# Kernel optimization log

Measured on AMD Instinct MI355X. Metric: run time of the kernel, lower is better.

## Reference

```python
import jax, jax.numpy as jnp
import numpy as np

N_PATHS = 8
T2_EFF = 0.5 * 100.0 + 0.5 * (100 // 50)  # p_dimer*T2_dimer + p_trimer*T2_trimer = 51.0
J_FREQ = 20.0


def setup_inputs() -> dict:
    key = jax.random.key(0)
    ks = jax.random.split(key, 5)
    B, D, H, P = 2048, 1024, 1024, N_PATHS
    return {
        "x": jax.random.normal(ks[0], (B, D), dtype=jnp.float32),
        "W_input": jax.random.normal(ks[1], (D, H), dtype=jnp.float32) * 0.1,
        "W_paths": jax.random.normal(ks[2], (P, H, H), dtype=jnp.float32) * 0.1,
        "J_coupling": jax.random.normal(ks[3], (P, P), dtype=jnp.float32) * 0.01,
        "coherent_state": jax.random.normal(ks[4], (B, P, H), dtype=jnp.float32),
        "t": jnp.ones((1,), dtype=jnp.float32),  # time_since_formation buffer
    }


def reference(x, W_input, W_paths, J_coupling, coherent_state, t):
    # base activation: [B, H]
    base = x @ W_input
    # all per-path matmuls batched into one einsum: [B, P, H]
    path_act = jnp.einsum("bh,phk->bpk", base, W_paths)
    # coherence decay gate (scalar, broadcasts)
    alpha = jnp.clip(jnp.exp(-t[0] / T2_EFF), 0.0, 1.0)
    superposition = alpha * coherent_state + (1.0 - alpha) * path_act
    # interference matrix from symmetrized J-coupling
    J_sym = 0.5 * (J_coupling + J_coupling.T)
    phase = 2.0 * jnp.pi * J_FREQ * t[0] / 1000.0
    interference = jax.nn.softmax(jnp.cos(phase * J_sym), axis=1)  # [P, P]
    # double-loop mixing == small matmul over path dim
    interfered = jnp.einsum("ij,bjh->bih", interference, superposition) / N_PATHS
    interfered = interfered * alpha  # coherence_factor == alpha
    # no measurement (default path): mean over paths
    return jnp.mean(interfered, axis=1)  # [B, H]
```

## Files before the change

kernel.cpp:

```cpp
#include <hip/hip_runtime.h>
#include <cstdint>


typedef __attribute__((ext_vector_type(8))) __bf16 bf16x8;
typedef __attribute__((ext_vector_type(4))) float f32x4;
typedef unsigned short u16;

__device__ __forceinline__ u16 f32_to_bf16_rne(float f) {
  unsigned int u = __float_as_uint(f);
  u += 0x7fffu + ((u >> 16) & 1u);
  return (u16)(u >> 16);
}

__device__ __forceinline__ f32x4 nt_load4(const float* p) {
  return __builtin_nontemporal_load((const f32x4*)p);
}

__device__ __forceinline__ void wave_scalars(const float* __restrict__ J,
                                             const float* __restrict__ t,
                                             float* w_out, float* alpha_out) {
  const int lane = threadIdx.x & 63;
  float tv = t[0];
  float alpha = fminf(fmaxf(expf(-tv / 51.0f), 0.0f), 1.0f);
  float phase = 2.0f * 3.14159265358979323846f * 20.0f * tv / 1000.0f;
  int i = lane >> 3, j = lane & 7;
  float jsym = 0.5f * (J[i * 8 + j] + J[j * 8 + i]);
  float e = expf(cosf(phase * jsym));
  float rs = e;
  rs += __shfl_xor(rs, 1);
  rs += __shfl_xor(rs, 2);
  rs += __shfl_xor(rs, 4);
  float p = e / rs;
  float cs = p;
  cs += __shfl_xor(cs, 8);
  cs += __shfl_xor(cs, 16);
  cs += __shfl_xor(cs, 32);
  *w_out = alpha * (1.0f / 64.0f) * cs;
  *alpha_out = alpha;
}

__global__ __launch_bounds__(256, 4) void k_prep(
    const float* __restrict__ x, const float* __restrict__ win,
    const float* __restrict__ wp, const float* __restrict__ J,
    const float* __restrict__ t, u16* __restrict__ xfrag,
    u16* __restrict__ winfrag, u16* __restrict__ wefrag) {
  __shared__ __align__(16) char smem[33024];
  const int blk = blockIdx.x;
  const int tid = threadIdx.x;
  const int lane = tid & 63;

  if (blk < 512) {
    float* lt = (float*)smem;
    float wv, alpha;
    wave_scalars(J, t, &wv, &alpha);
    float wLO[8];
#pragma unroll
    for (int p = 0; p < 8; p++)
      wLO[p] = __shfl(wv, (lane & 56) | p) * (1.0f - alpha);
    const int a0 = (blk & 31) * 32;
    const int b0 = (blk >> 5) * 64;
    f32x4 v[2][8];
#pragma unroll
    for (int s = 0; s < 2; s++) {
      const int item = s * 256 + tid;
      const int row = item >> 4, ch = item & 15;
      const float* base = wp + (size_t)(a0 + row) * 1024 + b0 + ch * 4;
#pragma unroll
      for (int j = 0; j < 8; j++) v[s][j] = nt_load4(base + (size_t)j * 1048576);
    }
#pragma unroll
    for (int s = 0; s < 2; s++) {
      const int item = s * 256 + tid;
      const int row = item >> 4, ch = item & 15;
      f32x4 acc = {0.f, 0.f, 0.f, 0.f};
#pragma unroll
      for (int j = 0; j < 8; j++) acc += wLO[j] * v[s][j];
      *(f32x4*)&lt[row * 68 + ch * 4] = acc;
    }
    __syncthreads();
    {
      const int lf = tid & 63, rtl = tid >> 6;
      const int rowh2 = rtl * 16 + (lf & 15);
      const int kh1 = (lf >> 4) << 3;
      __align__(16) u16 o[8];
#pragma unroll
      for (int i = 0; i < 8; i++)
        o[i] = f32_to_bf16_rne(lt[(kh1 + i) * 68 + rowh2]);
      const int rt = (b0 >> 4) + rtl, kt = a0 >> 5;
      *(uint4*)(wefrag + ((size_t)(rt * 32 + kt) * 64 + lf) * 8) = *(const uint4*)o;
    }
  } else {
    const int cid = blk - 512;
    const float* src;
    u16* dst;
    if (cid < 128) {
      src = x + (size_t)cid * 16384;
      dst = xfrag + (size_t)cid * 16384;
    } else {
      src = win + (size_t)(cid - 128) * 16384;
      dst = winfrag + (size_t)(cid - 128) * 16384;
    }
    u16* ld = (u16*)smem;
    f32x4 v[16];
#pragma unroll
    for (int row = 0; row < 16; row++) v[row] = nt_load4(src + row * 1024 + tid * 4);
#pragma unroll
    for (int row = 0; row < 16; row++) {
      ushort4 o;
      o.x = f32_to_bf16_rne(v[row][0]);
      o.y = f32_to_bf16_rne(v[row][1]);
      o.z = f32_to_bf16_rne(v[row][2]);
      o.w = f32_to_bf16_rne(v[row][3]);
      *(ushort4*)(ld + row * 1032 + tid * 4) = o;
    }
    __syncthreads();
#pragma unroll
    for (int s = 0; s < 8; s++) {
      int idx = s * 256 + tid;
      int lf = idx & 63, kt = idx >> 6;
      int row = lf & 15, colb = kt * 32 + ((lf >> 4) << 3);
      *(uint4*)(dst + (kt * 64 + lf) * 8) = *(const uint4*)(ld + row * 1032 + colb);
    }
  }
}

__global__ __launch_bounds__(256, 4) void k_gemm0(const u16* __restrict__ Af,
                                                  const u16* __restrict__ Bf,
                                                  u16* __restrict__ ofrag) {
  __shared__ u16 ct[64 * 36];
  const int tid = threadIdx.x;
  const int wave = tid >> 6, lane = tid & 63;
  const int quad = lane >> 4, t16 = lane & 15;
  const int m0 = blockIdx.x * 64;
  const int n0 = blockIdx.y * 32;
  const u16* ap = Af + ((size_t)((m0 + wave * 16) >> 4) * 32) * 512 + lane * 8;
  const u16* bp = Bf + ((size_t)(n0 >> 4) * 32) * 512 + lane * 8;

  f32x4 acc[2] = {{0.f, 0.f, 0.f, 0.f}, {0.f, 0.f, 0.f, 0.f}};
  for (int kb = 0; kb < 32; kb += 4) {
    bf16x8 a[4], b0[4], b1[4];
#pragma unroll
    for (int u = 0; u < 4; u++) {
      a[u] = *(const bf16x8*)(ap + (kb + u) * 512);
      b0[u] = *(const bf16x8*)(bp + (kb + u) * 512);
      b1[u] = *(const bf16x8*)(bp + (32 + kb + u) * 512);
    }
#pragma unroll
    for (int u = 0; u < 4; u++) {
      acc[0] = __builtin_amdgcn_mfma_f32_16x16x32_bf16(a[u], b0[u], acc[0], 0, 0, 0);
      acc[1] = __builtin_amdgcn_mfma_f32_16x16x32_bf16(a[u], b1[u], acc[1], 0, 0, 0);
    }
  }
#pragma unroll
  for (int r = 0; r < 4; r++)
#pragma unroll
    for (int ni = 0; ni < 2; ni++)
      ct[(wave * 16 + quad * 4 + r) * 36 + ni * 16 + t16] =
          f32_to_bf16_rne(acc[ni][r]);
  __syncthreads();
  {
    int lf = tid & 63, rtl = tid >> 6;
    int rowl = rtl * 16 + (lf & 15);
    int colb = (lf >> 4) << 3;
    __align__(16) u16 o[8];
#pragma unroll
    for (int i = 0; i < 8; i++) o[i] = ct[rowl * 36 + colb + i];
    *(uint4*)(ofrag +
              ((size_t)(((m0 >> 4) + rtl) * 32 + (n0 >> 5)) * 64 + lf) * 8) =
        *(const uint4*)o;
  }
}

__global__ __launch_bounds__(512, 4) void k_main(
    const u16* __restrict__ Af, const u16* __restrict__ Bf,
    const float* __restrict__ coh, const float* __restrict__ J,
    const float* __restrict__ t, float* __restrict__ out) {
  __shared__ float cs_lds[64 * 68];
  const int tid = threadIdx.x;
  const int wave = tid >> 6, lane = tid & 63;
  const int m0 = blockIdx.x * 64;
  const int n0 = blockIdx.y * 64;
  const int quad = lane >> 4, t16 = lane & 15;
  const int wm = (wave >> 1) * 32, wn = (wave & 1) * 32;

  f32x4 acc[2][2];
  if (wave < 4) {
    const u16* ap = Af + ((size_t)((m0 + wm) >> 4) * 32) * 512 + lane * 8;
    const u16* bp = Bf + ((size_t)((n0 + wn) >> 4) * 32) * 512 + lane * 8;
#pragma unroll
    for (int mi = 0; mi < 2; mi++)
#pragma unroll
      for (int ni = 0; ni < 2; ni++) acc[mi][ni] = (f32x4){0.f, 0.f, 0.f, 0.f};
    for (int kb = 0; kb < 32; kb += 4) {
      bf16x8 a0[4], a1[4], b0[4], b1[4];
#pragma unroll
      for (int u = 0; u < 4; u++) {
        a0[u] = *(const bf16x8*)(ap + (kb + u) * 512);
        a1[u] = *(const bf16x8*)(ap + (32 + kb + u) * 512);
        b0[u] = *(const bf16x8*)(bp + (kb + u) * 512);
        b1[u] = *(const bf16x8*)(bp + (32 + kb + u) * 512);
      }
#pragma unroll
      for (int u = 0; u < 4; u++) {
        acc[0][0] = __builtin_amdgcn_mfma_f32_16x16x32_bf16(a0[u], b0[u], acc[0][0], 0, 0, 0);
        acc[0][1] = __builtin_amdgcn_mfma_f32_16x16x32_bf16(a0[u], b1[u], acc[0][1], 0, 0, 0);
        acc[1][0] = __builtin_amdgcn_mfma_f32_16x16x32_bf16(a1[u], b0[u], acc[1][0], 0, 0, 0);
        acc[1][1] = __builtin_amdgcn_mfma_f32_16x16x32_bf16(a1[u], b1[u], acc[1][1], 0, 0, 0);
      }
    }
  } else {
    float wv, alpha;
    wave_scalars(J, t, &wv, &alpha);
    float wHI[8];
#pragma unroll
    for (int p = 0; p < 8; p++) wHI[p] = __shfl(wv, (lane & 56) | p) * alpha;
    const int tc = (wave - 4) * 64 + lane;
    const int c4 = tc & 15;
    const int rb = tc >> 4;
    const float* cb = coh + (size_t)m0 * 8192 + n0 + c4 * 4;
#pragma unroll
    for (int up = 0; up < 2; up++) {
      f32x4 v[2][8];
#pragma unroll
      for (int h = 0; h < 2; h++) {
        const float* cr = cb + (size_t)(rb + 16 * (up * 2 + h)) * 8192;
#pragma unroll
        for (int p = 0; p < 8; p++) v[h][p] = nt_load4(cr + p * 1024);
      }
#pragma unroll
      for (int h = 0; h < 2; h++) {
        f32x4 a4 = {0.f, 0.f, 0.f, 0.f};
#pragma unroll
        for (int p = 0; p < 8; p++) a4 += wHI[p] * v[h][p];
        *(f32x4*)&cs_lds[(rb + 16 * (up * 2 + h)) * 68 + c4 * 4] = a4;
      }
    }
  }
  __syncthreads();
  if (wave < 4) {
#pragma unroll
    for (int mi = 0; mi < 2; mi++)
#pragma unroll
      for (int r = 0; r < 4; r++) {
        const int ml = wm + mi * 16 + quad * 4 + r;
        const size_t mrow = (size_t)(m0 + ml) * 1024;
#pragma unroll
        for (int ni = 0; ni < 2; ni++) {
          const int nl = wn + ni * 16 + t16;
          out[mrow + n0 + nl] = acc[mi][ni][r] + cs_lds[ml * 68 + nl];
        }
      }
  }
}

extern "C" void kernel_launch(void* const* d_in, const int* in_sizes, int n_in,
                              void* d_out, int out_size, void* d_ws, size_t ws_size,
                              hipStream_t stream) {
  const float* x   = (const float*)d_in[0];
  const float* win = (const float*)d_in[1];
  const float* wp  = (const float*)d_in[2];
  const float* J   = (const float*)d_in[3];
  const float* coh = (const float*)d_in[4];
  const float* t   = (const float*)d_in[5];
  float* out = (float*)d_out;

  char* ws = (char*)d_ws;
  u16* xfrag   = (u16*)ws;
  u16* winfrag = (u16*)(ws + 4u * 1024 * 1024);
  u16* wefrag  = (u16*)(ws + 6u * 1024 * 1024);
  u16* wctfrag = (u16*)(ws + 8u * 1024 * 1024);

  k_prep<<<704, 256, 0, stream>>>(x, win, wp, J, t, xfrag, winfrag, wefrag);
  k_gemm0<<<dim3(16, 32), 256, 0, stream>>>(wefrag, winfrag, wctfrag);
  k_main<<<dim3(32, 16), 512, 0, stream>>>(xfrag, wctfrag, coh, J, t, out);
}
```

Measured before the change: 158.6 us.

## Move x conversion into gemm0 kernel and swizzle blocks across XCDs

New measurement: 157.1 us. About the same (-1.0%).

```diff
diff --git a/kernel.cpp b/kernel.cpp
--- a/kernel.cpp
+++ b/kernel.cpp
@@ -39,10 +39,34 @@
   *alpha_out = alpha;
 }
 
+__device__ __forceinline__ void convert16(const float* __restrict__ src,
+                                          u16* __restrict__ dst, u16* ld,
+                                          int tid) {
+  f32x4 v[16];
+#pragma unroll
+  for (int row = 0; row < 16; row++) v[row] = nt_load4(src + row * 1024 + tid * 4);
+#pragma unroll
+  for (int row = 0; row < 16; row++) {
+    ushort4 o;
+    o.x = f32_to_bf16_rne(v[row][0]);
+    o.y = f32_to_bf16_rne(v[row][1]);
+    o.z = f32_to_bf16_rne(v[row][2]);
+    o.w = f32_to_bf16_rne(v[row][3]);
+    *(ushort4*)(ld + row * 1032 + tid * 4) = o;
+  }
+  __syncthreads();
+#pragma unroll
+  for (int s = 0; s < 8; s++) {
+    int idx = s * 256 + tid;
+    int lf = idx & 63, kt = idx >> 6;
+    int row = lf & 15, colb = kt * 32 + ((lf >> 4) << 3);
+    *(uint4*)(dst + (kt * 64 + lf) * 8) = *(const uint4*)(ld + row * 1032 + colb);
+  }
+}
+
 __global__ __launch_bounds__(256, 4) void k_prep(
-    const float* __restrict__ x, const float* __restrict__ win,
-    const float* __restrict__ wp, const float* __restrict__ J,
-    const float* __restrict__ t, u16* __restrict__ xfrag,
+    const float* __restrict__ win, const float* __restrict__ wp,
+    const float* __restrict__ J, const float* __restrict__ t,
     u16* __restrict__ winfrag, u16* __restrict__ wefrag) {
   __shared__ __align__(16) char smem[33024];
   const int blk = blockIdx.x;
@@ -91,83 +115,66 @@
     }
   } else {
     const int cid = blk - 512;
-    const float* src;
-    u16* dst;
-    if (cid < 128) {
-      src = x + (size_t)cid * 16384;
-      dst = xfrag + (size_t)cid * 16384;
-    } else {
-      src = win + (size_t)(cid - 128) * 16384;
-      dst = winfrag + (size_t)(cid - 128) * 16384;
-    }
-    u16* ld = (u16*)smem;
-    f32x4 v[16];
-#pragma unroll
-    for (int row = 0; row < 16; row++) v[row] = nt_load4(src + row * 1024 + tid * 4);
-#pragma unroll
-    for (int row = 0; row < 16; row++) {
-      ushort4 o;
-      o.x = f32_to_bf16_rne(v[row][0]);
-      o.y = f32_to_bf16_rne(v[row][1]);
-      o.z = f32_to_bf16_rne(v[row][2]);
-      o.w = f32_to_bf16_rne(v[row][3]);
-      *(ushort4*)(ld + row * 1032 + tid * 4) = o;
-    }
+    convert16(win + (size_t)cid * 16384, winfrag + (size_t)cid * 16384,
+              (u16*)smem, tid);
+  }
+}
+
+__global__ __launch_bounds__(256, 4) void k_mid(
+    const float* __restrict__ x, const u16* __restrict__ Af,
+    const u16* __restrict__ Bf, u16* __restrict__ xfrag,
+    u16* __restrict__ ofrag) {
+  __shared__ __align__(16) char smem[33024];
+  const int blk = blockIdx.x;
+  const int tid = threadIdx.x;
+
+  if (blk < 512) {
+    u16* ct = (u16*)smem;
+    const int wave = tid >> 6, lane = tid & 63;
+    const int quad = lane >> 4, t16 = lane & 15;
+    const int xcd = blk & 7, i = blk >> 3;
+    const int m0 = (xcd + 8 * (i & 1)) * 64;
+    const int n0 = (i >> 1) * 32;
+    const u16* ap = Af + ((size_t)((m0 + wave * 16) >> 4) * 32) * 512 + lane * 8;
+    const u16* bp = Bf + ((size_t)(n0 >> 4) * 32) * 512 + lane * 8;
+
+    f32x4 acc[2] = {{0.f, 0.f, 0.f, 0.f}, {0.f, 0.f, 0.f, 0.f}};
+    for (int kb = 0; kb < 32; kb += 4) {
+      bf16x8 a[4], b0[4], b1[4];
+#pragma unroll
+      for (int u = 0; u < 4; u++) {
+        a[u] = *(const bf16x8*)(ap + (kb + u) * 512);
+        b0[u] = *(const bf16x8*)(bp + (kb + u) * 512);
+        b1[u] = *(const bf16x8*)(bp + (32 + kb + u) * 512);
+      }
+#pragma unroll
+      for (int u = 0; u < 4; u++) {
+        acc[0] = __builtin_amdgcn_mfma_f32_16x16x32_bf16(a[u], b0[u], acc[0], 0, 0, 0);
+        acc[1] = __builtin_amdgcn_mfma_f32_16x16x32_bf16(a[u], b1[u], acc[1], 0, 0, 0);
+      }
+    }
+#pragma unroll
+    for (int r = 0; r < 4; r++)
+#pragma unroll
+      for (int ni = 0; ni < 2; ni++)
+        ct[(wave * 16 + quad * 4 + r) * 36 + ni * 16 + t16] =
+            f32_to_bf16_rne(acc[ni][r]);
     __syncthreads();
-#pragma unroll
-    for (int s = 0; s < 8; s++) {
-      int idx = s * 256 + tid;
-      int lf = idx & 63, kt = idx >> 6;
-      int row = lf & 15, colb = kt * 32 + ((lf >> 4) << 3);
-      *(uint4*)(dst + (kt * 64 + lf) * 8) = *(const uint4*)(ld + row * 1032 + colb);
-    }
-  }
-}
-
-__global__ __launch_bounds__(256, 4) void k_gemm0(const u16* __restrict__ Af,
-                                                  const u16* __restrict__ Bf,
-                                                  u16* __restrict__ ofrag) {
-  __shared__ u16 ct[64 * 36];
-  const int tid = threadIdx.x;
-  const int wave = tid >> 6, lane = tid & 63;
-  const int quad = lane >> 4, t16 = lane & 15;
-  const int m0 = blockIdx.x * 64;
-  const int n0 = blockIdx.y * 32;
-  const u16* ap = Af + ((size_t)((m0 + wave * 16) >> 4) * 32) * 512 + lane * 8;
-  const u16* bp = Bf + ((size_t)(n0 >> 4) * 32) * 512 + lane * 8;
-
-  f32x4 acc[2] = {{0.f, 0.f, 0.f, 0.f}, {0.f, 0.f, 0.f, 0.f}};
-  for (int kb = 0; kb < 32; kb += 4) {
-    bf16x8 a[4], b0[4], b1[4];
-#pragma unroll
-    for (int u = 0; u < 4; u++) {
-      a[u] = *(const bf16x8*)(ap + (kb + u) * 512);
-      b0[u] = *(const bf16x8*)(bp + (kb + u) * 512);
-      b1[u] = *(const bf16x8*)(bp + (32 + kb + u) * 512);
-    }
-#pragma unroll
-    for (int u = 0; u < 4; u++) {
-      acc[0] = __builtin_amdgcn_mfma_f32_16x16x32_bf16(a[u], b0[u], acc[0], 0, 0, 0);
-      acc[1] = __builtin_amdgcn_mfma_f32_16x16x32_bf16(a[u], b1[u], acc[1], 0, 0, 0);
-    }
-  }
-#pragma unroll
-  for (int r = 0; r < 4; r++)
-#pragma unroll
-    for (int ni = 0; ni < 2; ni++)
-      ct[(wave * 16 + quad * 4 + r) * 36 + ni * 16 + t16] =
-          f32_to_bf16_rne(acc[ni][r]);
-  __syncthreads();
-  {
-    int lf = tid & 63, rtl = tid >> 6;
-    int rowl = rtl * 16 + (lf & 15);
-    int colb = (lf >> 4) << 3;
-    __align__(16) u16 o[8];
-#pragma unroll
-    for (int i = 0; i < 8; i++) o[i] = ct[rowl * 36 + colb + i];
-    *(uint4*)(ofrag +
-              ((size_t)(((m0 >> 4) + rtl) * 32 + (n0 >> 5)) * 64 + lf) * 8) =
-        *(const uint4*)o;
+    {
+      int lf = tid & 63, rtl = tid >> 6;
+      int rowl = rtl * 16 + (lf & 15);
+      int colb = (lf >> 4) << 3;
+      __align__(16) u16 o[8];
+#pragma unroll
+      for (int i2 = 0; i2 < 8; i2++) o[i2] = ct[rowl * 36 + colb + i2];
+      *(uint4*)(ofrag +
+                ((size_t)(((m0 >> 4) + rtl) * 32 + (n0 >> 5)) * 64 + lf) * 8) =
+          *(const uint4*)o;
+    }
+  } else {
+    const int cid = blk - 512;
+    convert16(x + (size_t)cid * 16384, xfrag + (size_t)cid * 16384, (u16*)smem,
+              tid);
   }
 }
 
@@ -178,8 +185,9 @@
   __shared__ float cs_lds[64 * 68];
   const int tid = threadIdx.x;
   const int wave = tid >> 6, lane = tid & 63;
-  const int m0 = blockIdx.x * 64;
-  const int n0 = blockIdx.y * 64;
+  const int xcd = blockIdx.x & 7, i = blockIdx.x >> 3;
+  const int m0 = (xcd + 8 * (i >> 4)) * 64;
+  const int n0 = (i & 15) * 64;
   const int quad = lane >> 4, t16 = lane & 15;
   const int wm = (wave >> 1) * 32, wn = (wave & 1) * 32;
 
@@ -270,7 +278,7 @@
   u16* wefrag  = (u16*)(ws + 6u * 1024 * 1024);
   u16* wctfrag = (u16*)(ws + 8u * 1024 * 1024);
 
-  k_prep<<<704, 256, 0, stream>>>(x, win, wp, J, t, xfrag, winfrag, wefrag);
-  k_gemm0<<<dim3(16, 32), 256, 0, stream>>>(wefrag, winfrag, wctfrag);
-  k_main<<<dim3(32, 16), 512, 0, stream>>>(xfrag, wctfrag, coh, J, t, out);
-}
+  k_prep<<<576, 256, 0, stream>>>(win, wp, J, t, winfrag, wefrag);
+  k_mid<<<640, 256, 0, stream>>>(x, wefrag, winfrag, xfrag, wctfrag);
+  k_main<<<512, 512, 0, stream>>>(xfrag, wctfrag, coh, J, t, out);
+}
```

## Fuse prep and both GEMMs into one persistent kernel with grid barriers

Applied to the files above, without the earlier changes.

New measurement: 354.7 us. 124% more time.

```diff
diff --git a/kernel.cpp b/kernel.cpp
--- a/kernel.cpp
+++ b/kernel.cpp
@@ -12,9 +12,7 @@
   return (u16)(u >> 16);
 }
 
-__device__ __forceinline__ f32x4 nt_load4(const float* p) {
-  return __builtin_nontemporal_load((const f32x4*)p);
-}
+__device__ __forceinline__ f32x4 ld4(const float* p) { return *(const f32x4*)p; }
 
 __device__ __forceinline__ void wave_scalars(const float* __restrict__ J,
                                              const float* __restrict__ t,
@@ -39,217 +37,229 @@
   *alpha_out = alpha;
 }
 
-__global__ __launch_bounds__(256, 4) void k_prep(
+__device__ __forceinline__ void grid_barrier(unsigned* cnt, unsigned target) {
+  __syncthreads();
+  __threadfence();
+  if (threadIdx.x == 0) {
+    __hip_atomic_fetch_add(cnt, 1u, __ATOMIC_ACQ_REL, __HIP_MEMORY_SCOPE_AGENT);
+    while (__hip_atomic_load(cnt, __ATOMIC_RELAXED, __HIP_MEMORY_SCOPE_AGENT) <
+           target)
+      __builtin_amdgcn_s_sleep(2);
+  }
+  __syncthreads();
+  __threadfence();
+}
+
+__global__ __launch_bounds__(512, 4) void k_fused(
     const float* __restrict__ x, const float* __restrict__ win,
     const float* __restrict__ wp, const float* __restrict__ J,
-    const float* __restrict__ t, u16* __restrict__ xfrag,
-    u16* __restrict__ winfrag, u16* __restrict__ wefrag) {
+    const float* __restrict__ t, const float* __restrict__ coh,
+    u16* __restrict__ xfrag, u16* __restrict__ winfrag,
+    u16* __restrict__ wefrag, u16* __restrict__ wctfrag,
+    float* __restrict__ out, unsigned* __restrict__ cnt) {
   __shared__ __align__(16) char smem[33024];
   const int blk = blockIdx.x;
   const int tid = threadIdx.x;
-  const int lane = tid & 63;
-
-  if (blk < 512) {
+  const int wave = tid >> 6, lane = tid & 63;
+  const int quad = lane >> 4, t16 = lane & 15;
+
+  float wv, alpha;
+  wave_scalars(J, t, &wv, &alpha);
+  float wLO[8], wHI[8];
+#pragma unroll
+  for (int p = 0; p < 8; p++) {
+    float wj = __shfl(wv, (lane & 56) | p);
+    wLO[p] = wj * (1.0f - alpha);
+    wHI[p] = wj * alpha;
+  }
+
+  {
     float* lt = (float*)smem;
-    float wv, alpha;
-    wave_scalars(J, t, &wv, &alpha);
-    float wLO[8];
-#pragma unroll
-    for (int p = 0; p < 8; p++)
-      wLO[p] = __shfl(wv, (lane & 56) | p) * (1.0f - alpha);
-    const int a0 = (blk & 31) * 32;
-    const int b0 = (blk >> 5) * 64;
+    const int row = tid >> 4, ch = tid & 15;
     f32x4 v[2][8];
 #pragma unroll
-    for (int s = 0; s < 2; s++) {
-      const int item = s * 256 + tid;
-      const int row = item >> 4, ch = item & 15;
+    for (int u = 0; u < 2; u++) {
+      const int tau = 2 * blk + u;
+      const int a0 = (tau & 31) * 32, b0 = (tau >> 5) * 64;
       const float* base = wp + (size_t)(a0 + row) * 1024 + b0 + ch * 4;
 #pragma unroll
-      for (int j = 0; j < 8; j++) v[s][j] = nt_load4(base + (size_t)j * 1048576);
-    }
-#pragma unroll
-    for (int s = 0; s < 2; s++) {
-      const int item = s * 256 + tid;
-      const int row = item >> 4, ch = item & 15;
+      for (int j = 0; j < 8; j++) v[u][j] = ld4(base + (size_t)j * 1048576);
+    }
+#pragma unroll
+    for (int u = 0; u < 2; u++) {
       f32x4 acc = {0.f, 0.f, 0.f, 0.f};
 #pragma unroll
-      for (int j = 0; j < 8; j++) acc += wLO[j] * v[s][j];
-      *(f32x4*)&lt[row * 68 + ch * 4] = acc;
+      for (int j = 0; j < 8; j++) acc += wLO[j] * v[u][j];
+      *(f32x4*)&lt[(u * 32 + row) * 68 + ch * 4] = acc;
     }
     __syncthreads();
     {
-      const int lf = tid & 63, rtl = tid >> 6;
+      const int u = tid >> 8, utid = tid & 255;
+      const int lf = utid & 63, rtl = utid >> 6;
+      const int tau = 2 * blk + u;
+      const int a0 = (tau & 31) * 32, b0 = (tau >> 5) * 64;
       const int rowh2 = rtl * 16 + (lf & 15);
       const int kh1 = (lf >> 4) << 3;
       __align__(16) u16 o[8];
 #pragma unroll
       for (int i = 0; i < 8; i++)
-        o[i] = f32_to_bf16_rne(lt[(kh1 + i) * 68 + rowh2]);
-      const int rt = (b0 >> 4) + rtl, kt = a0 >> 5;
-      *(uint4*)(wefrag + ((size_t)(rt * 32 + kt) * 64 + lf) * 8) = *(const uint4*)o;
-    }
-  } else {
-    const int cid = blk - 512;
+        o[i] = f32_to_bf16_rne(lt[(u * 32 + kh1 + i) * 68 + rowh2]);
+      *(uint4*)(wefrag +
+                ((size_t)(((b0 >> 4) + rtl) * 32 + (a0 >> 5)) * 64 + lf) * 8) =
+          *(const uint4*)o;
+    }
+    __syncthreads();
+  }
+
+  if (blk < 192) {
     const float* src;
     u16* dst;
-    if (cid < 128) {
-      src = x + (size_t)cid * 16384;
-      dst = xfrag + (size_t)cid * 16384;
+    if (blk < 128) {
+      src = x + (size_t)blk * 16384;
+      dst = xfrag + (size_t)blk * 16384;
     } else {
-      src = win + (size_t)(cid - 128) * 16384;
-      dst = winfrag + (size_t)(cid - 128) * 16384;
+      src = win + (size_t)(blk - 128) * 16384;
+      dst = winfrag + (size_t)(blk - 128) * 16384;
     }
     u16* ld = (u16*)smem;
-    f32x4 v[16];
-#pragma unroll
-    for (int row = 0; row < 16; row++) v[row] = nt_load4(src + row * 1024 + tid * 4);
-#pragma unroll
-    for (int row = 0; row < 16; row++) {
+    f32x4 v[8];
+#pragma unroll
+    for (int s = 0; s < 8; s++) {
+      int u2 = s * 512 + tid;
+      v[s] = ld4(src + (u2 >> 8) * 1024 + (u2 & 255) * 4);
+    }
+#pragma unroll
+    for (int s = 0; s < 8; s++) {
+      int u2 = s * 512 + tid;
       ushort4 o;
-      o.x = f32_to_bf16_rne(v[row][0]);
-      o.y = f32_to_bf16_rne(v[row][1]);
-      o.z = f32_to_bf16_rne(v[row][2]);
-      o.w = f32_to_bf16_rne(v[row][3]);
-      *(ushort4*)(ld + row * 1032 + tid * 4) = o;
-    }
-    __syncthreads();
-#pragma unroll
-    for (int s = 0; s < 8; s++) {
-      int idx = s * 256 + tid;
+      o.x = f32_to_bf16_rne(v[s][0]);
+      o.y = f32_to_bf16_rne(v[s][1]);
+      o.z = f32_to_bf16_rne(v[s][2]);
+      o.w = f32_to_bf16_rne(v[s][3]);
+      *(ushort4*)(ld + (u2 >> 8) * 1032 + (u2 & 255) * 4) = o;
+    }
+    __syncthreads();
+#pragma unroll
+    for (int s = 0; s < 4; s++) {
+      int idx = s * 512 + tid;
       int lf = idx & 63, kt = idx >> 6;
       int row = lf & 15, colb = kt * 32 + ((lf >> 4) << 3);
       *(uint4*)(dst + (kt * 64 + lf) * 8) = *(const uint4*)(ld + row * 1032 + colb);
     }
   }
-}
-
-__global__ __launch_bounds__(256, 4) void k_gemm0(const u16* __restrict__ Af,
-                                                  const u16* __restrict__ Bf,
-                                                  u16* __restrict__ ofrag) {
-  __shared__ u16 ct[64 * 36];
-  const int tid = threadIdx.x;
-  const int wave = tid >> 6, lane = tid & 63;
-  const int quad = lane >> 4, t16 = lane & 15;
-  const int m0 = blockIdx.x * 64;
-  const int n0 = blockIdx.y * 32;
-  const u16* ap = Af + ((size_t)((m0 + wave * 16) >> 4) * 32) * 512 + lane * 8;
-  const u16* bp = Bf + ((size_t)(n0 >> 4) * 32) * 512 + lane * 8;
-
-  f32x4 acc[2] = {{0.f, 0.f, 0.f, 0.f}, {0.f, 0.f, 0.f, 0.f}};
-  for (int kb = 0; kb < 32; kb += 4) {
-    bf16x8 a[4], b0[4], b1[4];
-#pragma unroll
-    for (int u = 0; u < 4; u++) {
-      a[u] = *(const bf16x8*)(ap + (kb + u) * 512);
-      b0[u] = *(const bf16x8*)(bp + (kb + u) * 512);
-      b1[u] = *(const bf16x8*)(bp + (32 + kb + u) * 512);
-    }
-#pragma unroll
-    for (int u = 0; u < 4; u++) {
-      acc[0] = __builtin_amdgcn_mfma_f32_16x16x32_bf16(a[u], b0[u], acc[0], 0, 0, 0);
-      acc[1] = __builtin_amdgcn_mfma_f32_16x16x32_bf16(a[u], b1[u], acc[1], 0, 0, 0);
-    }
-  }
-#pragma unroll
-  for (int r = 0; r < 4; r++)
-#pragma unroll
-    for (int ni = 0; ni < 2; ni++)
-      ct[(wave * 16 + quad * 4 + r) * 36 + ni * 16 + t16] =
-          f32_to_bf16_rne(acc[ni][r]);
-  __syncthreads();
+
+#pragma unroll
+  for (int half = 0; half < 2; half++) {
+    f32x4 v[2][8];
+    float* outp[2];
+#pragma unroll
+    for (int c = 0; c < 2; c++) {
+      const int cc = half * 2 + c;
+      const int u = cc >> 1, q = cc & 1;
+      const int tau = 2 * blk + u;
+      const int m0 = (tau >> 4) * 64, n0 = (tau & 15) * 64;
+      const int unit = q * 512 + tid;
+      const int row = unit >> 4, ch = unit & 15;
+      const float* cb = coh + (size_t)(m0 + row) * 8192 + n0 + ch * 4;
+#pragma unroll
+      for (int p = 0; p < 8; p++) v[c][p] = ld4(cb + p * 1024);
+      outp[c] = out + (size_t)(m0 + row) * 1024 + n0 + ch * 4;
+    }
+#pragma unroll
+    for (int c = 0; c < 2; c++) {
+      f32x4 a = {0.f, 0.f, 0.f, 0.f};
+#pragma unroll
+      for (int p = 0; p < 8; p++) a += wHI[p] * v[c][p];
+      *(f32x4*)outp[c] = a;
+    }
+  }
+
+  grid_barrier(cnt, 256);
+
   {
-    int lf = tid & 63, rtl = tid >> 6;
-    int rowl = rtl * 16 + (lf & 15);
-    int colb = (lf >> 4) << 3;
-    __align__(16) u16 o[8];
-#pragma unroll
-    for (int i = 0; i < 8; i++) o[i] = ct[rowl * 36 + colb + i];
-    *(uint4*)(ofrag +
-              ((size_t)(((m0 >> 4) + rtl) * 32 + (n0 >> 5)) * 64 + lf) * 8) =
-        *(const uint4*)o;
-  }
-}
-
-__global__ __launch_bounds__(512, 4) void k_main(
-    const u16* __restrict__ Af, const u16* __restrict__ Bf,
-    const float* __restrict__ coh, const float* __restrict__ J,
-    const float* __restrict__ t, float* __restrict__ out) {
-  __shared__ float cs_lds[64 * 68];
-  const int tid = threadIdx.x;
-  const int wave = tid >> 6, lane = tid & 63;
-  const int m0 = blockIdx.x * 64;
-  const int n0 = blockIdx.y * 64;
-  const int quad = lane >> 4, t16 = lane & 15;
-  const int wm = (wave >> 1) * 32, wn = (wave & 1) * 32;
-
-  f32x4 acc[2][2];
-  if (wave < 4) {
-    const u16* ap = Af + ((size_t)((m0 + wm) >> 4) * 32) * 512 + lane * 8;
-    const u16* bp = Bf + ((size_t)((n0 + wn) >> 4) * 32) * 512 + lane * 8;
-#pragma unroll
-    for (int mi = 0; mi < 2; mi++)
-#pragma unroll
-      for (int ni = 0; ni < 2; ni++) acc[mi][ni] = (f32x4){0.f, 0.f, 0.f, 0.f};
+    const int m0 = (blk & 15) * 64;
+    const int n0 = (blk >> 4) * 64 + (wave >> 2) * 32;
+    const int uw = wave & 3;
+    const u16* ap = wefrag + ((size_t)((m0 + uw * 16) >> 4) * 32) * 512 + lane * 8;
+    const u16* bp = winfrag + ((size_t)(n0 >> 4) * 32) * 512 + lane * 8;
+    f32x4 acc[2] = {{0.f, 0.f, 0.f, 0.f}, {0.f, 0.f, 0.f, 0.f}};
     for (int kb = 0; kb < 32; kb += 4) {
-      bf16x8 a0[4], a1[4], b0[4], b1[4];
+      bf16x8 a[4], b0[4], b1[4];
 #pragma unroll
       for (int u = 0; u < 4; u++) {
-        a0[u] = *(const bf16x8*)(ap + (kb + u) * 512);
-        a1[u] = *(const bf16x8*)(ap + (32 + kb + u) * 512);
+        a[u] = *(const bf16x8*)(ap + (kb + u) * 512);
         b0[u] = *(const bf16x8*)(bp + (kb + u) * 512);
         b1[u] = *(const bf16x8*)(bp + (32 + kb + u) * 512);
       }
 #pragma unroll
       for (int u = 0; u < 4; u++) {
-        acc[0][0] = __builtin_amdgcn_mfma_f32_16x16x32_bf16(a0[u], b0[u], acc[0][0], 0, 0, 0);
-        acc[0][1] = __builtin_amdgcn_mfma_f32_16x16x32_bf16(a0[u], b1[u], acc[0][1], 0, 0, 0);
-        acc[1][0] = __builtin_amdgcn_mfma_f32_16x16x32_bf16(a1[u], b0[u], acc[1][0], 0, 0, 0);
-        acc[1][1] = __builtin_amdgcn_mfma_f32_16x16x32_bf16(a1[u], b1[u], acc[1][1], 0, 0, 0);
+        acc[0] = __builtin_amdgcn_mfma_f32_16x16x32_bf16(a[u], b0[u], acc[0], 0, 0, 0);
+        acc[1] = __builtin_amdgcn_mfma_f32_16x16x32_bf16(a[u], b1[u], acc[1], 0, 0, 0);
       }
     }
-  } else {
-    float wv, alpha;
-    wave_scalars(J, t, &wv, &alpha);
-    float wHI[8];
-#pragma unroll
-    for (int p = 0; p < 8; p++) wHI[p] = __shfl(wv, (lane & 56) | p) * alpha;
-    const int tc = (wave - 4) * 64 + lane;
-    const int c4 = tc & 15;
-    const int rb = tc >> 4;
-    const float* cb = coh + (size_t)m0 * 8192 + n0 + c4 * 4;
-#pragma unroll
-    for (int up = 0; up < 2; up++) {
-      f32x4 v[2][8];
-#pragma unroll
-      for (int h = 0; h < 2; h++) {
-        const float* cr = cb + (size_t)(rb + 16 * (up * 2 + h)) * 8192;
-#pragma unroll
-        for (int p = 0; p < 8; p++) v[h][p] = nt_load4(cr + p * 1024);
-      }
-#pragma unroll
-      for (int h = 0; h < 2; h++) {
-        f32x4 a4 = {0.f, 0.f, 0.f, 0.f};
-#pragma unroll
-        for (int p = 0; p < 8; p++) a4 += wHI[p] * v[h][p];
-        *(f32x4*)&cs_lds[(rb + 16 * (up * 2 + h)) * 68 + c4 * 4] = a4;
-      }
-    }
-  }
-  __syncthreads();
-  if (wave < 4) {
-#pragma unroll
-    for (int mi = 0; mi < 2; mi++)
-#pragma unroll
-      for (int r = 0; r < 4; r++) {
-        const int ml = wm + mi * 16 + quad * 4 + r;
-        const size_t mrow = (size_t)(m0 + ml) * 1024;
-#pragma unroll
-        for (int ni = 0; ni < 2; ni++) {
-          const int nl = wn + ni * 16 + t16;
-          out[mrow + n0 + nl] = acc[mi][ni][r] + cs_lds[ml * 68 + nl];
+    u16* ct = (u16*)smem;
+    u16* ctu = ct + (wave >> 2) * 64 * 36;
+#pragma unroll
+    for (int r = 0; r < 4; r++)
+#pragma unroll
+      for (int ni = 0; ni < 2; ni++)
+        ctu[(uw * 16 + quad * 4 + r) * 36 + ni * 16 + t16] =
+            f32_to_bf16_rne(acc[ni][r]);
+    __syncthreads();
+    {
+      const int ug = tid >> 8, utid = tid & 255;
+      const int n0u = (blk >> 4) * 64 + ug * 32;
+      const int lf = utid & 63, rtl = utid >> 6;
+      const int rowl = rtl * 16 + (lf & 15), colb = (lf >> 4) << 3;
+      const u16* ctg = ct + ug * 64 * 36;
+      __align__(16) u16 o[8];
+#pragma unroll
+      for (int i = 0; i < 8; i++) o[i] = ctg[rowl * 36 + colb + i];
+      *(uint4*)(wctfrag +
+                ((size_t)(((m0 >> 4) + rtl) * 32 + (n0u >> 5)) * 64 + lf) * 8) =
+          *(const uint4*)o;
+    }
+  }
+
+  grid_barrier(cnt, 512);
+
+  {
+    const int wm = (wave >> 2) * 32, wn = (wave & 3) * 16;
+#pragma unroll
+    for (int u = 0; u < 2; u++) {
+      const int tau = 2 * blk + u;
+      const int m0 = (tau >> 4) * 64, n0 = (tau & 15) * 64;
+      const u16* ap = xfrag + ((size_t)((m0 + wm) >> 4) * 32) * 512 + lane * 8;
+      const u16* bp = wctfrag + ((size_t)((n0 + wn) >> 4) * 32) * 512 + lane * 8;
+      float cpre[2][4];
+#pragma unroll
+      for (int mi = 0; mi < 2; mi++)
+#pragma unroll
+        for (int r = 0; r < 4; r++)
+          cpre[mi][r] =
+              out[(size_t)(m0 + wm + mi * 16 + quad * 4 + r) * 1024 + n0 + wn + t16];
+      f32x4 acc[2] = {{0.f, 0.f, 0.f, 0.f}, {0.f, 0.f, 0.f, 0.f}};
+      for (int kb = 0; kb < 32; kb += 4) {
+        bf16x8 a0[4], a1[4], b[4];
+#pragma unroll
+        for (int uu = 0; uu < 4; uu++) {
+          a0[uu] = *(const bf16x8*)(ap + (kb + uu) * 512);
+          a1[uu] = *(const bf16x8*)(ap + (32 + kb + uu) * 512);
+          b[uu] = *(const bf16x8*)(bp + (kb + uu) * 512);
+        }
+#pragma unroll
+        for (int uu = 0; uu < 4; uu++) {
+          acc[0] = __builtin_amdgcn_mfma_f32_16x16x32_bf16(a0[uu], b[uu], acc[0], 0, 0, 0);
+          acc[1] = __builtin_amdgcn_mfma_f32_16x16x32_bf16(a1[uu], b[uu], acc[1], 0, 0, 0);
         }
       }
+#pragma unroll
+      for (int mi = 0; mi < 2; mi++)
+#pragma unroll
+        for (int r = 0; r < 4; r++)
+          out[(size_t)(m0 + wm + mi * 16 + quad * 4 + r) * 1024 + n0 + wn + t16] =
+              acc[mi][r] + cpre[mi][r];
+    }
   }
 }
 
@@ -269,8 +279,9 @@
   u16* winfrag = (u16*)(ws + 4u * 1024 * 1024);
   u16* wefrag  = (u16*)(ws + 6u * 1024 * 1024);
   u16* wctfrag = (u16*)(ws + 8u * 1024 * 1024);
-
-  k_prep<<<704, 256, 0, stream>>>(x, win, wp, J, t, xfrag, winfrag, wefrag);
-  k_gemm0<<<dim3(16, 32), 256, 0, stream>>>(wefrag, winfrag, wctfrag);
-  k_main<<<dim3(32, 16), 512, 0, stream>>>(xfrag, wctfrag, coh, J, t, out);
-}
+  unsigned* cnt = (unsigned*)(ws + 12u * 1024 * 1024);
+
+  hipMemsetAsync(cnt, 0, 64, stream);
+  k_fused<<<256, 512, 0, stream>>>(x, win, wp, J, t, coh, xfrag, winfrag,
+                                   wefrag, wctfrag, out, cnt);
+}
```
